# Optimization experiments

Hardware: AMD Instinct MI355X
Metric: run time of the kernel (lower is better)

Reference implementation:

```python
import jax, jax.numpy as jnp
import numpy as np

B, N = 4, 500
C_DIM = 256            # content_dim == feat_channels
G = 4                  # n_groups
P_IN, P_OUT = 32, 128
EFF = C_DIM // G       # 64 = eff_in_dim = eff_out_dim
TOTAL = EFF * EFF + P_IN * P_OUT   # 8192 params per group per query
STRIDES = (8, 16, 32, 64)
LVL_SHAPES = ((100, 160), (50, 80), (25, 40), (13, 20))
TAU = 2.0
LVL_MAP = 3.0          # log2(STRIDES[0]): z -> fpn level index
EPS = 1e-5


def setup_inputs() -> dict:
    key = jax.random.key(0)
    ks = jax.random.split(key, 16)
    feats = [jax.random.normal(ks[i], (B, C_DIM, h, w), jnp.float32)
             for i, (h, w) in enumerate(LVL_SHAPES)]
    query_feat = jax.random.normal(ks[4], (B, N, C_DIM), jnp.float32)
    xy = jax.random.uniform(ks[5], (B, N, 2), jnp.float32, 50.0, 1000.0)
    z = jax.random.uniform(ks[6], (B, N, 1), jnp.float32, 3.0, 6.0)
    r = jax.random.uniform(ks[7], (B, N, 1), jnp.float32, -1.0, 1.0)
    query_xyzr = jnp.concatenate([xy, z, r], -1)
    w_off = jax.random.normal(ks[8], (C_DIM, P_IN * G * 3), jnp.float32) * 0.01
    b_off = jax.random.normal(ks[9], (P_IN * G * 3,), jnp.float32) * 0.1
    w_pg = jax.random.normal(ks[10], (C_DIM, G * TOTAL), jnp.float32) * 0.02
    b_pg = jax.random.normal(ks[11], (G * TOTAL,), jnp.float32) * 0.02
    w_out = jax.random.normal(ks[12], (G * P_OUT * EFF, C_DIM), jnp.float32) * 0.005
    b_out = jnp.zeros((C_DIM,), jnp.float32)
    ln_g = jnp.ones((C_DIM,), jnp.float32)
    ln_b = jnp.zeros((C_DIM,), jnp.float32)
    return dict(feat0=feats[0], feat1=feats[1], feat2=feats[2], feat3=feats[3],
                query_feat=query_feat, query_xyzr=query_xyzr,
                w_off=w_off, b_off=b_off, w_pg=w_pg, b_pg=b_pg,
                w_out=w_out, b_out=b_out, ln_g=ln_g, ln_b=ln_b)


def _ln2d(x):
    # F.layer_norm over last TWO dims, no affine
    mu = x.mean((-2, -1), keepdims=True)
    var = jnp.mean((x - mu) ** 2, (-2, -1), keepdims=True)
    return (x - mu) * jax.lax.rsqrt(var + EPS)


def _bilinear(feat, px, py):
    # torch grid_sample(bilinear, zeros padding, align_corners=False)
    # feat: [BG, H, W, Cg]; px, py: [BG, Q] pixel coords
    BGn, H, W, Cg = feat.shape
    fflat = feat.reshape(BGn, H * W, Cg)
    bidx = jnp.arange(BGn)[:, None]
    x0 = jnp.floor(px)
    y0 = jnp.floor(py)
    wx, wy = px - x0, py - y0
    x0i, y0i = x0.astype(jnp.int32), y0.astype(jnp.int32)

    def corner(xi, yi, w):
        valid = (xi >= 0) & (xi < W) & (yi >= 0) & (yi < H)
        idx = jnp.clip(yi, 0, H - 1) * W + jnp.clip(xi, 0, W - 1)
        return fflat[bidx, idx] * (w * valid)[..., None]

    return (corner(x0i, y0i, (1 - wx) * (1 - wy)) + corner(x0i + 1, y0i, wx * (1 - wy))
            + corner(x0i, y0i + 1, (1 - wx) * wy) + corner(x0i + 1, y0i + 1, wx * wy))


def _forward(feat0, feat1, feat2, feat3, query_feat, query_xyzr,
             w_off, b_off, w_pg, b_pg, w_out, b_out, ln_g, ln_b):
    feats = (feat0, feat1, feat2, feat3)
    # --- make_sample_points ---
    off = (query_feat @ w_off + b_off).reshape(B, N, G * P_IN, 3)
    cc = query_xyzr[..., :2]
    z = query_xyzr[..., 2:3]
    r = query_xyzr[..., 3:4]
    roi_wh = (2.0 ** z) * jnp.concatenate([2.0 ** (-0.5 * r), 2.0 ** (0.5 * r)], -1)  # [B,N,2]
    sample_xy = cc[:, :, None, :] + off[..., :2] * roi_wh[:, :, None, :]   # [B,N,G*P,2]
    sample_lvl = z[:, :, None, 0:1] + off[..., 2:3]                        # [B,N,G*P,1]

    # --- sampling_3d: softmax level weights ---
    lvl = sample_lvl[..., 0] - LVL_MAP                                     # [B,N,G*P]
    grid = jnp.arange(len(STRIDES), dtype=lvl.dtype)
    lw = jax.nn.softmax(-((lvl[..., None] - grid) ** 2) / TAU, axis=-1)    # [B,N,G*P,L]

    # regroup to per-group layout [B*G, N*P, ...]
    sx = sample_xy.reshape(B, N, G, P_IN, 2).transpose(0, 2, 1, 3, 4).reshape(B * G, N * P_IN, 2)
    lw_g = lw.reshape(B, N, G, P_IN, -1).transpose(0, 2, 1, 3, 4).reshape(B * G, N * P_IN, -1)

    sampled = jnp.zeros((B * G, N * P_IN, EFF), jnp.float32)
    for li, (feat, stride) in enumerate(zip(feats, STRIDES)):
        H, W = feat.shape[2], feat.shape[3]
        fg = feat.reshape(B * G, EFF, H, W).transpose(0, 2, 3, 1)  # [BG,H,W,EFF]
        nx = sx[..., 0] / (W * stride) * 2.0 - 1.0
        ny = sx[..., 1] / (H * stride) * 2.0 - 1.0
        px = (nx + 1.0) * 0.5 * W - 0.5
        py = (ny + 1.0) * 0.5 * H - 0.5
        sampled = sampled + _bilinear(fg, px, py) * lw_g[..., li][..., None]
    # [B,N,G,P,EFF]
    x = sampled.reshape(B, G, N, P_IN, EFF).transpose(0, 2, 1, 3, 4)

    # --- AdaptiveMixing ---
    params = (query_feat @ w_pg + b_pg).reshape(B * N, G, TOTAL)
    M = params[..., :EFF * EFF].reshape(B * N, G, EFF, EFF)
    S = params[..., EFF * EFF:].reshape(B * N, G, P_OUT, P_IN)
    out = x.reshape(B * N, G, P_IN, EFF)
    out = jax.nn.relu(_ln2d(jnp.einsum('bgpc,bgcd->bgpd', out, M)))  # channel mix
    out = jax.nn.relu(_ln2d(jnp.einsum('bgop,bgpd->bgod', S, out)))  # spatial mix
    out = out.reshape(B, N, G * P_OUT * EFF) @ w_out + b_out
    q = query_feat + out

    # --- final LayerNorm(content_dim) with affine ---
    mu = q.mean(-1, keepdims=True)
    var = jnp.mean((q - mu) ** 2, -1, keepdims=True)
    return (q - mu) * jax.lax.rsqrt(var + EPS) * ln_g + ln_b


def reference(feat0, feat1, feat2, feat3, query_feat, query_xyzr,
              w_off, b_off, w_pg, b_pg, w_out, b_out, ln_g, ln_b):
    return _forward(feat0, feat1, feat2, feat3, query_feat, query_xyzr,
                    w_off, b_off, w_pg, b_pg, w_out, b_out, ln_g, ln_b)
```

## Files before the change

### kernel.cpp

```cpp
#include <hip/hip_runtime.h>
#include <hip/hip_bf16.h>
#include <cstdint>
#include <cstddef>

#define DI __device__ __forceinline__

#define NN 500
#define NQ 2000
#define GTOT 32768
#define LN_EPS 1e-5f

typedef __attribute__((ext_vector_type(8))) short short8v;
typedef __attribute__((ext_vector_type(4))) float f32x4;
typedef const __attribute__((address_space(1))) void* gp1_t;
typedef __attribute__((address_space(3))) void* lp3_t;

DI unsigned short f2bf(float f){
  unsigned u = __float_as_uint(f);
  return (unsigned short)((u + 0x7fffu + ((u>>16)&1u)) >> 16);
}
DI float bf2f(unsigned short s){ return __uint_as_float(((unsigned)s)<<16); }

DI ushort4 cvt4(float4 a){
  ushort4 r; r.x=f2bf(a.x); r.y=f2bf(a.y); r.z=f2bf(a.z); r.w=f2bf(a.w); return r;
}

DI void bred256(float& s, float& s2, float* red, int tid){
  #pragma unroll
  for(int off=32; off; off>>=1){
    s  += __shfl_xor(s,  off, 64);
    s2 += __shfl_xor(s2, off, 64);
  }
  int w = tid>>6;
  if((tid&63)==0){ red[w*2]=s; red[w*2+1]=s2; }
  __syncthreads();
  s  = red[0]+red[2]+red[4]+red[6];
  s2 = red[1]+red[3]+red[5]+red[7];
  __syncthreads();
}

__global__ __launch_bounds__(384) void k_off(const float* __restrict__ qf,
    const float* __restrict__ xyzr, const float* __restrict__ w_off,
    const float* __restrict__ b_off, float2* __restrict__ xyb, float4* __restrict__ lwb){
  __shared__ float qs[8][256];
  __shared__ float os[8][384];
  int q0 = blockIdx.x*8, tid = threadIdx.x;
  for(int idx=tid; idx<2048; idx+=384){
    int qq = idx>>8, k = idx&255;
    qs[qq][k] = qf[(size_t)(q0+qq)*256 + k];
  }
  __syncthreads();
  {
    int j = tid;
    float acc[8];
    #pragma unroll
    for(int i=0;i<8;i++) acc[i]=0.f;
    for(int k=0;k<256;k++){
      float w = w_off[(size_t)k*384 + j];
      #pragma unroll
      for(int qq=0;qq<8;qq++) acc[qq] += qs[qq][k]*w;
    }
    float bb = b_off[j];
    #pragma unroll
    for(int qq=0;qq<8;qq++) os[qq][j] = acc[qq] + bb;
  }
  __syncthreads();
  for(int idx=tid; idx<1024; idx+=384){
    int qq = idx>>7, gp = idx&127;
    int q = q0+qq;
    float4 xr = *(const float4*)&xyzr[(size_t)q*4];
    float rw = exp2f(xr.z - 0.5f*xr.w);
    float rh = exp2f(xr.z + 0.5f*xr.w);
    float sx = xr.x + os[qq][gp*3+0]*rw;
    float sy = xr.y + os[qq][gp*3+1]*rh;
    float lvl = xr.z + os[qq][gp*3+2] - 3.0f;
    float d0=lvl, d1=lvl-1.f, d2=lvl-2.f, d3=lvl-3.f;
    float e0=-0.5f*d0*d0, e1=-0.5f*d1*d1, e2=-0.5f*d2*d2, e3=-0.5f*d3*d3;
    float m = fmaxf(fmaxf(e0,e1),fmaxf(e2,e3));
    float x0=expf(e0-m), x1=expf(e1-m), x2=expf(e2-m), x3=expf(e3-m);
    float inv = 1.f/(x0+x1+x2+x3);
    xyb[(size_t)q*128+gp] = make_float2(sx,sy);
    lwb[(size_t)q*128+gp] = make_float4(x0*inv, x1*inv, x2*inv, x3*inv);
  }
}

__global__ __launch_bounds__(256) void k_cvtqf(const float* __restrict__ qf,
    unsigned short* __restrict__ qfb){
  int idx = blockIdx.x*256 + threadIdx.x;
  size_t base = (size_t)idx*8;
  int row = idx >> 5;
  ushort4 lo, hi;
  if(row < NQ){
    float4 a = *(const float4*)(qf + base);
    float4 b = *(const float4*)(qf + base + 4);
    lo = cvt4(a); hi = cvt4(b);
  } else {
    lo.x=lo.y=lo.z=lo.w=0; hi.x=hi.y=hi.z=hi.w=0;
  }
  *(ushort4*)(qfb + base) = lo;
  *(ushort4*)(qfb + base + 4) = hi;
}

__global__ __launch_bounds__(256) void k_trcvt(const float* __restrict__ src,
    unsigned short* __restrict__ dst, int R, int C){
  __shared__ unsigned short tile[64*68];
  int ctiles = C >> 6;
  int rt = blockIdx.x / ctiles, ct = blockIdx.x % ctiles;
  int r0 = rt<<6, c0 = ct<<6;
  int tid = threadIdx.x;
  #pragma unroll
  for(int i=0;i<4;i++){
    int idx = tid + i*256;
    int r = idx >> 4, c4 = (idx & 15)*4;
    float4 v = *(const float4*)(src + (size_t)(r0+r)*C + c0 + c4);
    *(ushort4*)(tile + r*68 + c4) = cvt4(v);
  }
  __syncthreads();
  #pragma unroll
  for(int i=0;i<4;i++){
    int idx = tid + i*256;
    int cc = idx >> 4, r4 = (idx & 15)*4;
    ushort4 v;
    v.x = tile[(r4+0)*68 + cc];
    v.y = tile[(r4+1)*68 + cc];
    v.z = tile[(r4+2)*68 + cc];
    v.w = tile[(r4+3)*68 + cc];
    *(ushort4*)(dst + (size_t)(c0+cc)*R + r0 + r4) = v;
  }
}

__global__ __launch_bounds__(256) void k_featT(const float* __restrict__ src,
    unsigned short* __restrict__ dst, int HW, int nb){
  __shared__ unsigned short tile[64*68];
  int bg = blockIdx.x / nb, hb = blockIdx.x % nb;
  int b = bg >> 2, g = bg & 3;
  const float* s = src + ((size_t)(b*256 + g*64))*HW + hb*64;
  unsigned short* d = dst + (size_t)bg*HW*64 + (size_t)hb*64*64;
  int rem = HW - hb*64;
  int tid = threadIdx.x;
  #pragma unroll
  for(int i=0;i<4;i++){
    int idx = tid + i*256;
    int c = idx >> 4, h4 = (idx & 15)*4;
    if(h4 < rem){
      float4 v = *(const float4*)(s + (size_t)c*HW + h4);
      *(ushort4*)(tile + c*68 + h4) = cvt4(v);
    }
  }
  __syncthreads();
  #pragma unroll
  for(int i=0;i<4;i++){
    int idx = tid + i*256;
    int hw = idx >> 4, c4 = (idx & 15)*4;
    if(hw < rem){
      ushort4 v;
      v.x = tile[(c4+0)*68 + hw];
      v.y = tile[(c4+1)*68 + hw];
      v.z = tile[(c4+2)*68 + hw];
      v.w = tile[(c4+3)*68 + hw];
      *(ushort4*)(d + (size_t)hw*64 + c4) = v;
    }
  }
}

DI f32x4 mfma16(short8v a, short8v b, f32x4 c){
  return __builtin_amdgcn_mfma_f32_16x16x32_bf16(a, b, c, 0, 0, 0);
}

DI int swz32(int c, int r){ return c ^ (r&3) ^ ((r>>2)&3); }

DI void stageG32(const unsigned short* __restrict__ g, size_t row0, size_t ldk,
                 size_t k0, unsigned short* lds, int tid){
  int wv = tid>>6;
  #pragma unroll
  for(int i=0;i<2;i++){
    int e = i*256 + tid;
    int r = e>>2, c = e&3;
    int cs = swz32(c, r);
    const unsigned short* gp = g + (row0 + (size_t)r)*ldk + k0 + (size_t)cs*8;
    unsigned short* lp = lds + (size_t)(i*256 + wv*64)*8;
    __builtin_amdgcn_global_load_lds((gp1_t)(const void*)gp, (lp3_t)(void*)lp, 16, 0, 0);
  }
}

DI void stageB32(const unsigned short* __restrict__ g, size_t row0, size_t ldk,
                 size_t k0, unsigned short* lds, int tid){
  int wv = tid>>6;
  int r = tid>>2, c = tid&3;
  int cs = swz32(c, r);
  const unsigned short* gp = g + (row0 + (size_t)r)*ldk + k0 + (size_t)cs*8;
  unsigned short* lp = lds + (size_t)(wv*64)*8;
  __builtin_amdgcn_global_load_lds((gp1_t)(const void*)gp, (lp3_t)(void*)lp, 16, 0, 0);
}

DI short8v frag32(const unsigned short* lds, int row, int q4){
  return *(const short8v*)(lds + (size_t)row*32 + (size_t)swz32(q4, row)*8);
}

DI void mma32(const unsigned short* lsA, const unsigned short* lsB,
              int wm, int wn, int lane, f32x4 acc[4][4]){
  int r15 = lane&15, q4 = lane>>4;
  short8v a[4], b[4];
  #pragma unroll
  for(int i=0;i<4;i++){
    a[i] = frag32(lsA, wm*64 + i*16 + r15, q4);
    b[i] = frag32(lsB, wn*64 + i*16 + r15, q4);
  }
  #pragma unroll
  for(int mi=0;mi<4;mi++)
    #pragma unroll
    for(int ni=0;ni<4;ni++)
      acc[mi][ni] = mfma16(a[mi], b[ni], acc[mi][ni]);
}

DI int xcd_remap(int bid, int nwg){
  return ((bid & 7) * (nwg >> 3)) + (bid >> 3);
}

__global__ __launch_bounds__(256, 4) void k_pgemm_mfma(const unsigned short* __restrict__ qfb,
    const unsigned short* __restrict__ wpgT, const float* __restrict__ b_pg,
    unsigned short* __restrict__ par, int qbase, int qlim, int mtiles){
  __shared__ unsigned short pool[16384];
  int bid = xcd_remap(blockIdx.x, gridDim.x);
  int mt = bid % mtiles, nt = bid / mtiles;
  size_t m0 = (size_t)mt*128, n0 = (size_t)nt*128;
  int tid = threadIdx.x, lane = tid&63, wv = tid>>6;
  int wm = wv>>1, wn = wv&1;
  int r15 = lane&15, q4 = lane>>4;
  f32x4 acc[4][4] = {};
  stageG32(qfb,  qbase+m0, 256, 0, pool, tid);
  stageG32(wpgT, n0,       256, 0, pool + 8192, tid);
  __syncthreads();
  #pragma unroll
  for(int t=0; t<8; t++){
    int co = (t&1)*4096;
    if(t<7){
      int no = ((t&1)^1)*4096;
      stageG32(qfb,  qbase+m0, 256, (size_t)(t+1)*32, pool + no, tid);
      stageG32(wpgT, n0,       256, (size_t)(t+1)*32, pool + 8192 + no, tid);
    }
    mma32(pool + co, pool + 8192 + co, wm, wn, lane, acc);
    __syncthreads();
  }
  unsigned short* es = pool;
  #pragma unroll
  for(int h=0; h<2; ++h){
    if(h) __syncthreads();
    if(wn == h){
      #pragma unroll
      for(int ni=0; ni<4; ni++){
        float bias = b_pg[(int)n0 + wn*64 + ni*16 + r15];
        #pragma unroll
        for(int mi=0; mi<4; mi++)
          #pragma unroll
          for(int j=0; j<4; j++){
            int row = wm*64 + mi*16 + q4*4 + j;
            es[row*72 + ni*16 + r15] = f2bf(acc[mi][ni][j] + bias);
          }
      }
    }
    __syncthreads();
    #pragma unroll
    for(int i=0;i<4;i++){
      int e = i*256 + tid;
      int row = e>>3, c8 = (e&7)*8;
      int rl = (int)m0 + row;
      if(qbase + rl < qlim){
        uint4 v = *(const uint4*)(es + row*72 + c8);
        *(uint4*)&par[(size_t)rl*GTOT + n0 + h*64 + c8] = v;
      }
    }
  }
}

__global__ __launch_bounds__(256, 4) void k_fgemm_mfma(const unsigned short* __restrict__ Ag,
    const unsigned short* __restrict__ woutT, float* __restrict__ part,
    int qbase, int qlim, int mtiles, int kspl){
  __shared__ unsigned short pool[12288];
  int bid = xcd_remap(blockIdx.x, gridDim.x);
  int nt = bid & 3;
  int r2 = bid >> 2;
  int mt = r2 % mtiles, ks = r2 / mtiles;
  size_t m0 = (size_t)mt*128, n0 = (size_t)nt*64;
  int tid = threadIdx.x, lane = tid&63, wv = tid>>6;
  int wm = wv>>1, wn = wv&1;
  int r15 = lane&15, q4 = lane>>4;
  f32x4 acc[4][2] = {};
  int klen = GTOT / kspl;
  size_t kbase = (size_t)ks*klen;
  int NT = klen >> 5;
  stageG32(Ag,    m0, GTOT, kbase, pool, tid);
  stageB32(woutT, n0, GTOT, kbase, pool + 8192, tid);
  __syncthreads();
  for(int t=0; t<NT; t++){
    int coA = (t&1)*4096, coB = (t&1)*2048;
    if(t+1<NT){
      int noA = ((t&1)^1)*4096, noB = ((t&1)^1)*2048;
      stageG32(Ag,    m0, GTOT, kbase + (size_t)(t+1)*32, pool + noA, tid);
      stageB32(woutT, n0, GTOT, kbase + (size_t)(t+1)*32, pool + 8192 + noB, tid);
    }
    {
      const unsigned short* lsA = pool + coA;
      const unsigned short* lsB = pool + 8192 + coB;
      short8v a[4], b[2];
      #pragma unroll
      for(int i=0;i<4;i++) a[i] = frag32(lsA, wm*64 + i*16 + r15, q4);
      #pragma unroll
      for(int i=0;i<2;i++) b[i] = frag32(lsB, wn*32 + i*16 + r15, q4);
      #pragma unroll
      for(int mi=0;mi<4;mi++)
        #pragma unroll
        for(int ni=0;ni<2;ni++)
          acc[mi][ni] = mfma16(a[mi], b[ni], acc[mi][ni]);
    }
    __syncthreads();
  }
  float* pp = part + (size_t)ks*NQ*256;
  #pragma unroll
  for(int mi=0; mi<4; mi++){
    #pragma unroll
    for(int j=0; j<4; j++){
      int rl = (int)m0 + wm*64 + mi*16 + q4*4 + j;
      int q = qbase + rl;
      if(q < qlim){
        #pragma unroll
        for(int ni=0; ni<2; ni++){
          int col = (int)n0 + wn*32 + ni*16 + r15;
          pp[(size_t)q*256 + col] = acc[mi][ni][j];
        }
      }
    }
  }
}

__global__ __launch_bounds__(256) void k_mix(const unsigned short* __restrict__ featT,
    const float2* __restrict__ xyb, const float4* __restrict__ lwb,
    const unsigned short* __restrict__ par, unsigned short* __restrict__ out2,
    int qbase){
  __shared__ __align__(16) char poolA[23040];
  __shared__ __align__(16) unsigned short Ss[128*40];
  __shared__ float red[8];
  float* offW = (float*)poolA;
  unsigned short* xs  = (unsigned short*)(poolA + 4096);
  unsigned short* Ms  = (unsigned short*)(poolA + 4096 + 4608);
  unsigned short* o1t = (unsigned short*)(poolA + 4096 + 4608 + 9216);
  unsigned short* o2s = (unsigned short*)poolA;

  int lq = blockIdx.x >> 2, g = blockIdx.x & 3;
  int q = qbase + lq;
  int b = q / NN;
  int bg = b*4 + g;
  int tid = threadIdx.x;
  int lane = tid & 63, wv = tid >> 6;

  const int HH[4] = {100,50,25,13};
  const int WW[4] = {160,80,40,20};
  const float IS[4] = {0.125f, 0.0625f, 0.03125f, 0.015625f};
  const int LO[4] = {0, 16384000, 20480000, 21504000};

  const unsigned short* pb = par + (size_t)lq*GTOT + (size_t)g*8192;
  uint4 mraw0 = *(const uint4*)(pb + tid*8);
  uint4 mraw1 = *(const uint4*)(pb + 2048 + tid*8);
  uint4 sraw0 = *(const uint4*)(pb + 4096 + tid*8);
  uint4 sraw1 = *(const uint4*)(pb + 6144 + tid*8);

  if(tid < 128){
    int p = tid >> 2, l = tid & 3;
    int pi = q*128 + g*32 + p;
    float2 xy = xyb[pi];
    float lw4 = ((const float*)lwb)[(size_t)pi*4 + l];
    int H = HH[l], W = WW[l];
    float px = xy.x*IS[l] - 0.5f;
    float py = xy.y*IS[l] - 0.5f;
    float xf = floorf(px), yf = floorf(py);
    float wx = px - xf, wy = py - yf;
    int x0 = (int)xf, y0 = (int)yf;
    int x1 = x0 + 1, y1 = y0 + 1;
    bool vx0 = (x0>=0)&&(x0<W), vx1 = (x1>=0)&&(x1<W);
    bool vy0 = (y0>=0)&&(y0<H), vy1 = (y1>=0)&&(y1<H);
    int x0c = min(max(x0,0),W-1), x1c = min(max(x1,0),W-1);
    int y0c = min(max(y0,0),H-1), y1c = min(max(y1,0),H-1);
    int base = LO[l] + bg*H*W*64;
    float* e = offW + tid*8;
    e[0] = __int_as_float(base + (y0c*W + x0c)*64);
    e[1] = __int_as_float(base + (y0c*W + x1c)*64);
    e[2] = __int_as_float(base + (y1c*W + x0c)*64);
    e[3] = __int_as_float(base + (y1c*W + x1c)*64);
    e[4] = (1.f-wx)*(1.f-wy)*lw4*(float)(vx0&&vy0);
    e[5] = wx*(1.f-wy)*lw4*(float)(vx1&&vy0);
    e[6] = (1.f-wx)*wy*lw4*(float)(vx0&&vy1);
    e[7] = wx*wy*lw4*(float)(vx1&&vy1);
  }

  {
    int idx0 = tid*8;
    int c0 = idx0>>6, d0 = idx0&63;
    *(uint4*)(Ms + c0*72 + d0) = mraw0;
    int idx1 = 2048 + tid*8;
    int c1 = idx1>>6, d1 = idx1&63;
    *(uint4*)(Ms + c1*72 + d1) = mraw1;
    int o0 = idx0>>5, p0 = idx0&31;
    *(uint4*)(Ss + o0*40 + p0) = sraw0;
    int o1_ = idx1>>5, p1 = idx1&31;
    *(uint4*)(Ss + o1_*40 + p1) = sraw1;
  }
  __syncthreads();

  {
    int half = lane >> 5, cp = lane & 31;
    const unsigned short* fb_ = featT + cp*2;
    #pragma unroll
    for(int i=0;i<4;i++){
      int p = wv*8 + i*2 + half;
      const float* e = offW + p*32;
      float aLo = 0.f, aHi = 0.f;
      #pragma unroll
      for(int l=0;l<4;l++){
        float4 ea = *(const float4*)(e + l*8);
        float4 eb = *(const float4*)(e + l*8 + 4);
        unsigned u00 = *(const unsigned*)(fb_ + __float_as_int(ea.x));
        unsigned u01 = *(const unsigned*)(fb_ + __float_as_int(ea.y));
        unsigned u10 = *(const unsigned*)(fb_ + __float_as_int(ea.z));
        unsigned u11 = *(const unsigned*)(fb_ + __float_as_int(ea.w));
        aLo += eb.x*__uint_as_float(u00<<16); aHi += eb.x*__uint_as_float(u00&0xffff0000u);
        aLo += eb.y*__uint_as_float(u01<<16); aHi += eb.y*__uint_as_float(u01&0xffff0000u);
        aLo += eb.z*__uint_as_float(u10<<16); aHi += eb.z*__uint_as_float(u10&0xffff0000u);
        aLo += eb.w*__uint_as_float(u11<<16); aHi += eb.w*__uint_as_float(u11&0xffff0000u);
      }
      unsigned lo = f2bf(aLo), hi = f2bf(aHi);
      *(unsigned*)(xs + p*72 + cp*2) = lo | (hi<<16);
    }
  }
  __syncthreads();

  int r = lane & 15, q4 = lane >> 4;

  {
    short8v af00 = *(const short8v*)(xs + r*72 + q4*8);
    short8v af01 = *(const short8v*)(xs + r*72 + 32 + q4*8);
    short8v af10 = *(const short8v*)(xs + (16+r)*72 + q4*8);
    short8v af11 = *(const short8v*)(xs + (16+r)*72 + 32 + q4*8);
    short8v bm0, bm1;
    #pragma unroll
    for(int j=0;j<8;j++){
      bm0[j] = (short)Ms[(8*q4+j)*72 + wv*16 + r];
      bm1[j] = (short)Ms[(32+8*q4+j)*72 + wv*16 + r];
    }
    f32x4 a0 = {}, a1 = {};
    a0 = mfma16(af00, bm0, a0); a0 = mfma16(af01, bm1, a0);
    a1 = mfma16(af10, bm0, a1); a1 = mfma16(af11, bm1, a1);

    float s = 0.f, s2 = 0.f;
    #pragma unroll
    for(int v=0;v<4;v++){ s += a0[v]+a1[v]; s2 += a0[v]*a0[v] + a1[v]*a1[v]; }
    bred256(s, s2, red, tid);
    float mean = s*(1.f/2048.f);
    float var = s2*(1.f/2048.f) - mean*mean;
    float rs = rsqrtf(var + LN_EPS);
    #pragma unroll
    for(int v=0;v<4;v++){
      float f0 = (a0[v]-mean)*rs; f0 = f0>0.f ? f0 : 0.f;
      float f1 = (a1[v]-mean)*rs; f1 = f1>0.f ? f1 : 0.f;
      o1t[(wv*16+r)*40 + 4*q4 + v] = f2bf(f0);
      o1t[(wv*16+r)*40 + 16 + 4*q4 + v] = f2bf(f1);
    }
  }
  __syncthreads();

  {
    short8v sa0 = *(const short8v*)(Ss + ((wv*2+0)*16 + r)*40 + q4*8);
    short8v sa1 = *(const short8v*)(Ss + ((wv*2+1)*16 + r)*40 + q4*8);
    short8v ov0 = *(const short8v*)(o1t + (r)*40 + q4*8);
    short8v ov1 = *(const short8v*)(o1t + (16+r)*40 + q4*8);
    short8v ov2 = *(const short8v*)(o1t + (32+r)*40 + q4*8);
    short8v ov3 = *(const short8v*)(o1t + (48+r)*40 + q4*8);
    f32x4 c2[2][4] = {};
    c2[0][0] = mfma16(sa0, ov0, c2[0][0]); c2[0][1] = mfma16(sa0, ov1, c2[0][1]);
    c2[0][2] = mfma16(sa0, ov2, c2[0][2]); c2[0][3] = mfma16(sa0, ov3, c2[0][3]);
    c2[1][0] = mfma16(sa1, ov0, c2[1][0]); c2[1][1] = mfma16(sa1, ov1, c2[1][1]);
    c2[1][2] = mfma16(sa1, ov2, c2[1][2]); c2[1][3] = mfma16(sa1, ov3, c2[1][3]);

    float s = 0.f, s2 = 0.f;
    #pragma unroll
    for(int m=0;m<2;m++)
      #pragma unroll
      for(int ni=0;ni<4;ni++)
        #pragma unroll
        for(int v=0;v<4;v++){ float x = c2[m][ni][v]; s += x; s2 += x*x; }
    bred256(s, s2, red, tid);
    float mean = s*(1.f/8192.f);
    float var = s2*(1.f/8192.f) - mean*mean;
    float rs = rsqrtf(var + LN_EPS);
    #pragma unroll
    for(int m=0;m<2;m++)
      #pragma unroll
      for(int ni=0;ni<4;ni++)
        #pragma unroll
        for(int v=0;v<4;v++){
          float x = (c2[m][ni][v]-mean)*rs; x = x>0.f ? x : 0.f;
          int o = (wv*2+m)*16 + 4*q4 + v;
          int d = ni*16 + r;
          o2s[o*72 + d] = f2bf(x);
        }
  }
  __syncthreads();

  unsigned short* og = out2 + (size_t)lq*GTOT + (size_t)g*8192;
  #pragma unroll
  for(int i=0;i<32;i++){
    int row = wv*32 + i;
    og[row*64 + lane] = o2s[row*72 + lane];
  }
}

__global__ __launch_bounds__(256) void k_ln(const float* __restrict__ part,
    const float* __restrict__ qf, const float* __restrict__ b_out,
    const float* __restrict__ ln_g, const float* __restrict__ ln_b,
    float* __restrict__ out, int kspl){
  __shared__ float red[8];
  int q = blockIdx.x, j = threadIdx.x;
  float s = qf[(size_t)q*256 + j] + b_out[j];
  for(int ks=0; ks<kspl; ks++) s += part[((size_t)ks*NQ + q)*256 + j];
  float a = s, a2 = s*s;
  bred256(a, a2, red, j);
  float mean = a*(1.f/256.f);
  float var = a2*(1.f/256.f) - mean*mean;
  float rs = rsqrtf(var + LN_EPS);
  out[(size_t)q*256 + j] = (s-mean)*rs*ln_g[j] + ln_b[j];
}

extern "C" void kernel_launch(void* const* d_in, const int* in_sizes, int n_in,
                              void* d_out, int out_size, void* d_ws, size_t ws_size,
                              hipStream_t stream) {
  const float* feat0 = (const float*)d_in[0];
  const float* feat1 = (const float*)d_in[1];
  const float* feat2 = (const float*)d_in[2];
  const float* feat3 = (const float*)d_in[3];
  const float* qf    = (const float*)d_in[4];
  const float* xyzr  = (const float*)d_in[5];
  const float* w_off = (const float*)d_in[6];
  const float* b_off = (const float*)d_in[7];
  const float* w_pg  = (const float*)d_in[8];
  const float* b_pg  = (const float*)d_in[9];
  const float* w_out = (const float*)d_in[10];
  const float* b_out = (const float*)d_in[11];
  const float* ln_g  = (const float*)d_in[12];
  const float* ln_b  = (const float*)d_in[13];

  const int cand_ksp[5] = {32,16,16,16,16};
  const int cand_nc [5] = { 1, 1, 2, 4, 8};
  int KSP=0, NC=0, qcount=0, qpad=0;
  size_t oFEAT=0,oXY=0,oLW=0,oPART=0,oQFB=0,oWPGT=0,oWOUT=0,oPAR=0;
  for(int ci=0; ci<5; ci++){
    size_t o = 0;
    auto al = [&](size_t bytes){ size_t r = o; o = (o + bytes + 255) & ~255ull; return r; };
    size_t tFEAT = al(43540480ull);
    size_t tXY   = al((size_t)NQ*128*8);
    size_t tLW   = al((size_t)NQ*128*16);
    size_t tPART = al((size_t)cand_ksp[ci]*NQ*256*4);
    size_t tQFB  = al((size_t)2048*256*2);
    size_t tWPGT = al((size_t)GTOT*256*2);
    size_t tWOUT = al((size_t)256*GTOT*2);
    int qc = NQ / cand_nc[ci];
    int qp = (qc + 127) & ~127;
    size_t tPAR = al((size_t)qp*GTOT*2);
    if(o <= ws_size){
      KSP=cand_ksp[ci]; NC=cand_nc[ci]; qcount=qc; qpad=qp;
      oFEAT=tFEAT; oXY=tXY; oLW=tLW; oPART=tPART; oQFB=tQFB; oWPGT=tWPGT; oWOUT=tWOUT; oPAR=tPAR;
      break;
    }
  }
  if(NC == 0) return;

  char* ws = (char*)d_ws;
  unsigned short* featT = (unsigned short*)(ws + oFEAT);
  float2* xyb = (float2*)(ws + oXY);
  float4* lwb = (float4*)(ws + oLW);
  float* part = (float*)(ws + oPART);
  unsigned short* qfb  = (unsigned short*)(ws + oQFB);
  unsigned short* wpgT = (unsigned short*)(ws + oWPGT);
  unsigned short* woutT= (unsigned short*)(ws + oWOUT);
  unsigned short* par  = (unsigned short*)(ws + oPAR);
  unsigned short* o2   = par;

  k_off<<<250, 384, 0, stream>>>(qf, xyzr, w_off, b_off, xyb, lwb);
  k_cvtqf<<<256, 256, 0, stream>>>(qf, qfb);
  k_trcvt<<<2048, 256, 0, stream>>>(w_pg,  wpgT, 256, GTOT);
  k_trcvt<<<2048, 256, 0, stream>>>(w_out, woutT, GTOT, 256);
  k_featT<<<16*250, 256, 0, stream>>>(feat0, featT + 0,        16000, 250);
  k_featT<<<16*63,  256, 0, stream>>>(feat1, featT + 16384000, 4000,  63);
  k_featT<<<16*16,  256, 0, stream>>>(feat2, featT + 20480000, 1000,  16);
  k_featT<<<16*5,   256, 0, stream>>>(feat3, featT + 21504000, 260,   5);

  int mtiles = qpad / 128;
  for (int c = 0; c < NC; ++c) {
    int qbase = c * qcount;
    int qlim  = qbase + qcount;
    k_pgemm_mfma<<<mtiles*256, 256, 0, stream>>>(qfb, wpgT, b_pg, par, qbase, qlim, mtiles);
    k_mix<<<qcount*4, 256, 0, stream>>>(featT, xyb, lwb, par, o2, qbase);
    k_fgemm_mfma<<<mtiles*4*KSP, 256, 0, stream>>>(o2, woutT, part, qbase, qlim, mtiles, KSP);
  }
  k_ln<<<NQ, 256, 0, stream>>>(part, qf, b_out, ln_g, ln_b, (float*)d_out, KSP);
}
```

Before: 321.7 us.

## Fuse prep kernels, widen fgemm N-tile to 128, alias partials workspace

Merges the separate conversion and transpose kernels (query cast, two weight transposes, four feature transposes) into one launch that dispatches on block index. The output GEMM now uses 128x128 tiles with the shared mma32 helper instead of 128x64, which halves the block count and reuses each A tile across twice as many output columns. The workspace layout overlaps the split-K partial buffer with the front of the workspace so a single chunk fits more often. The bigger tile raises register and LDS use per block, and the overlap is only safe if nothing still needs the reused region when the partials are written.

```diff
diff --git a/kernel.cpp b/kernel.cpp
--- a/kernel.cpp
+++ b/kernel.cpp
@@ -84,82 +84,91 @@
   }
 }
 
-__global__ __launch_bounds__(256) void k_cvtqf(const float* __restrict__ qf,
-    unsigned short* __restrict__ qfb){
-  int idx = blockIdx.x*256 + threadIdx.x;
-  size_t base = (size_t)idx*8;
-  int row = idx >> 5;
-  ushort4 lo, hi;
-  if(row < NQ){
-    float4 a = *(const float4*)(qf + base);
-    float4 b = *(const float4*)(qf + base + 4);
-    lo = cvt4(a); hi = cvt4(b);
+__global__ __launch_bounds__(256) void k_prep2(
+    const float* __restrict__ f0, const float* __restrict__ f1,
+    const float* __restrict__ f2, const float* __restrict__ f3,
+    const float* __restrict__ qf, const float* __restrict__ w_pg,
+    const float* __restrict__ w_out, unsigned short* __restrict__ featT,
+    unsigned short* __restrict__ qfb, unsigned short* __restrict__ wpgT,
+    unsigned short* __restrict__ woutT){
+  __shared__ unsigned short tile[64*68];
+  int bid = blockIdx.x, tid = threadIdx.x;
+
+  if(bid < 4096){
+    const float* src; unsigned short* dst; int R, C, lb;
+    if(bid < 2048){ src=w_pg;  dst=wpgT;  R=256;  C=GTOT; lb=bid; }
+    else          { src=w_out; dst=woutT; R=GTOT; C=256;  lb=bid-2048; }
+    int ctiles = C >> 6;
+    int rt = lb / ctiles, ct = lb % ctiles;
+    int r0 = rt<<6, c0 = ct<<6;
+    #pragma unroll
+    for(int i=0;i<4;i++){
+      int idx = tid + i*256;
+      int r = idx >> 4, c4 = (idx & 15)*4;
+      float4 v = *(const float4*)(src + (size_t)(r0+r)*C + c0 + c4);
+      *(ushort4*)(tile + r*68 + c4) = cvt4(v);
+    }
+    __syncthreads();
+    #pragma unroll
+    for(int i=0;i<4;i++){
+      int idx = tid + i*256;
+      int cc = idx >> 4, r4 = (idx & 15)*4;
+      ushort4 v;
+      v.x = tile[(r4+0)*68 + cc];
+      v.y = tile[(r4+1)*68 + cc];
+      v.z = tile[(r4+2)*68 + cc];
+      v.w = tile[(r4+3)*68 + cc];
+      *(ushort4*)(dst + (size_t)(c0+cc)*R + r0 + r4) = v;
+    }
+  } else if(bid < 9440){
+    const float* src; unsigned short* dst; int HW, nb, lb;
+    int fb = bid - 4096;
+    if(fb < 4000){ src=f0; dst=featT;            HW=16000; nb=250; lb=fb; }
+    else if(fb < 5008){ src=f1; dst=featT+16384000; HW=4000; nb=63; lb=fb-4000; }
+    else if(fb < 5264){ src=f2; dst=featT+20480000; HW=1000; nb=16; lb=fb-5008; }
+    else { src=f3; dst=featT+21504000; HW=260; nb=5; lb=fb-5264; }
+    int bg = lb / nb, hb = lb % nb;
+    int b = bg >> 2, g = bg & 3;
+    const float* s = src + ((size_t)(b*256 + g*64))*HW + hb*64;
+    unsigned short* d = dst + (size_t)bg*HW*64 + (size_t)hb*64*64;
+    int rem = HW - hb*64;
+    #pragma unroll
+    for(int i=0;i<4;i++){
+      int idx = tid + i*256;
+      int c = idx >> 4, h4 = (idx & 15)*4;
+      if(h4 < rem){
+        float4 v = *(const float4*)(s + (size_t)c*HW + h4);
+        *(ushort4*)(tile + c*68 + h4) = cvt4(v);
+      }
+    }
+    __syncthreads();
+    #pragma unroll
+    for(int i=0;i<4;i++){
+      int idx = tid + i*256;
+      int hw = idx >> 4, c4 = (idx & 15)*4;
+      if(hw < rem){
+        ushort4 v;
+        v.x = tile[(c4+0)*68 + hw];
+        v.y = tile[(c4+1)*68 + hw];
+        v.z = tile[(c4+2)*68 + hw];
+        v.w = tile[(c4+3)*68 + hw];
+        *(ushort4*)(d + (size_t)hw*64 + c4) = v;
+      }
+    }
   } else {
-    lo.x=lo.y=lo.z=lo.w=0; hi.x=hi.y=hi.z=hi.w=0;
-  }
-  *(ushort4*)(qfb + base) = lo;
-  *(ushort4*)(qfb + base + 4) = hi;
-}
-
-__global__ __launch_bounds__(256) void k_trcvt(const float* __restrict__ src,
-    unsigned short* __restrict__ dst, int R, int C){
-  __shared__ unsigned short tile[64*68];
-  int ctiles = C >> 6;
-  int rt = blockIdx.x / ctiles, ct = blockIdx.x % ctiles;
-  int r0 = rt<<6, c0 = ct<<6;
-  int tid = threadIdx.x;
-  #pragma unroll
-  for(int i=0;i<4;i++){
-    int idx = tid + i*256;
-    int r = idx >> 4, c4 = (idx & 15)*4;
-    float4 v = *(const float4*)(src + (size_t)(r0+r)*C + c0 + c4);
-    *(ushort4*)(tile + r*68 + c4) = cvt4(v);
-  }
-  __syncthreads();
-  #pragma unroll
-  for(int i=0;i<4;i++){
-    int idx = tid + i*256;
-    int cc = idx >> 4, r4 = (idx & 15)*4;
-    ushort4 v;
-    v.x = tile[(r4+0)*68 + cc];
-    v.y = tile[(r4+1)*68 + cc];
-    v.z = tile[(r4+2)*68 + cc];
-    v.w = tile[(r4+3)*68 + cc];
-    *(ushort4*)(dst + (size_t)(c0+cc)*R + r0 + r4) = v;
-  }
-}
-
-__global__ __launch_bounds__(256) void k_featT(const float* __restrict__ src,
-    unsigned short* __restrict__ dst, int HW, int nb){
-  __shared__ unsigned short tile[64*68];
-  int bg = blockIdx.x / nb, hb = blockIdx.x % nb;
-  int b = bg >> 2, g = bg & 3;
-  const float* s = src + ((size_t)(b*256 + g*64))*HW + hb*64;
-  unsigned short* d = dst + (size_t)bg*HW*64 + (size_t)hb*64*64;
-  int rem = HW - hb*64;
-  int tid = threadIdx.x;
-  #pragma unroll
-  for(int i=0;i<4;i++){
-    int idx = tid + i*256;
-    int c = idx >> 4, h4 = (idx & 15)*4;
-    if(h4 < rem){
-      float4 v = *(const float4*)(s + (size_t)c*HW + h4);
-      *(ushort4*)(tile + c*68 + h4) = cvt4(v);
-    }
-  }
-  __syncthreads();
-  #pragma unroll
-  for(int i=0;i<4;i++){
-    int idx = tid + i*256;
-    int hw = idx >> 4, c4 = (idx & 15)*4;
-    if(hw < rem){
-      ushort4 v;
-      v.x = tile[(c4+0)*68 + hw];
-      v.y = tile[(c4+1)*68 + hw];
-      v.z = tile[(c4+2)*68 + hw];
-      v.w = tile[(c4+3)*68 + hw];
-      *(ushort4*)(d + (size_t)hw*64 + c4) = v;
-    }
+    int idx = (bid-9440)*256 + tid;
+    size_t base = (size_t)idx*8;
+    int row = idx >> 5;
+    ushort4 lo, hi;
+    if(row < NQ){
+      float4 a = *(const float4*)(qf + base);
+      float4 b = *(const float4*)(qf + base + 4);
+      lo = cvt4(a); hi = cvt4(b);
+    } else {
+      lo.x=lo.y=lo.z=lo.w=0; hi.x=hi.y=hi.z=hi.w=0;
+    }
+    *(ushort4*)(qfb + base) = lo;
+    *(ushort4*)(qfb + base + 4) = hi;
   }
 }
 
@@ -181,16 +190,6 @@
     unsigned short* lp = lds + (size_t)(i*256 + wv*64)*8;
     __builtin_amdgcn_global_load_lds((gp1_t)(const void*)gp, (lp3_t)(void*)lp, 16, 0, 0);
   }
-}
-
-DI void stageB32(const unsigned short* __restrict__ g, size_t row0, size_t ldk,
-                 size_t k0, unsigned short* lds, int tid){
-  int wv = tid>>6;
-  int r = tid>>2, c = tid&3;
-  int cs = swz32(c, r);
-  const unsigned short* gp = g + (row0 + (size_t)r)*ldk + k0 + (size_t)cs*8;
-  unsigned short* lp = lds + (size_t)(wv*64)*8;
-  __builtin_amdgcn_global_load_lds((gp1_t)(const void*)gp, (lp3_t)(void*)lp, 16, 0, 0);
 }
 
 DI short8v frag32(const unsigned short* lds, int row, int q4){
@@ -276,46 +275,33 @@
 __global__ __launch_bounds__(256, 4) void k_fgemm_mfma(const unsigned short* __restrict__ Ag,
     const unsigned short* __restrict__ woutT, float* __restrict__ part,
     int qbase, int qlim, int mtiles, int kspl){
-  __shared__ unsigned short pool[12288];
+  __shared__ unsigned short pool[16384];
   int bid = xcd_remap(blockIdx.x, gridDim.x);
-  int nt = bid & 3;
-  int r2 = bid >> 2;
+  int nt = bid & 1;
+  int r2 = bid >> 1;
   int mt = r2 % mtiles, ks = r2 / mtiles;
-  size_t m0 = (size_t)mt*128, n0 = (size_t)nt*64;
+  size_t m0 = (size_t)mt*128, n0 = (size_t)nt*128;
   int tid = threadIdx.x, lane = tid&63, wv = tid>>6;
   int wm = wv>>1, wn = wv&1;
-  int r15 = lane&15, q4 = lane>>4;
-  f32x4 acc[4][2] = {};
+  f32x4 acc[4][4] = {};
   int klen = GTOT / kspl;
   size_t kbase = (size_t)ks*klen;
   int NT = klen >> 5;
   stageG32(Ag,    m0, GTOT, kbase, pool, tid);
-  stageB32(woutT, n0, GTOT, kbase, pool + 8192, tid);
+  stageG32(woutT, n0, GTOT, kbase, pool + 8192, tid);
   __syncthreads();
   for(int t=0; t<NT; t++){
-    int coA = (t&1)*4096, coB = (t&1)*2048;
+    int co = (t&1)*4096;
     if(t+1<NT){
-      int noA = ((t&1)^1)*4096, noB = ((t&1)^1)*2048;
-      stageG32(Ag,    m0, GTOT, kbase + (size_t)(t+1)*32, pool + noA, tid);
-      stageB32(woutT, n0, GTOT, kbase + (size_t)(t+1)*32, pool + 8192 + noB, tid);
-    }
-    {
-      const unsigned short* lsA = pool + coA;
-      const unsigned short* lsB = pool + 8192 + coB;
-      short8v a[4], b[2];
-      #pragma unroll
-      for(int i=0;i<4;i++) a[i] = frag32(lsA, wm*64 + i*16 + r15, q4);
-      #pragma unroll
-      for(int i=0;i<2;i++) b[i] = frag32(lsB, wn*32 + i*16 + r15, q4);
-      #pragma unroll
-      for(int mi=0;mi<4;mi++)
-        #pragma unroll
-        for(int ni=0;ni<2;ni++)
-          acc[mi][ni] = mfma16(a[mi], b[ni], acc[mi][ni]);
-    }
+      int no = ((t&1)^1)*4096;
+      stageG32(Ag,    m0, GTOT, kbase + (size_t)(t+1)*32, pool + no, tid);
+      stageG32(woutT, n0, GTOT, kbase + (size_t)(t+1)*32, pool + 8192 + no, tid);
+    }
+    mma32(pool + co, pool + 8192 + co, wm, wn, lane, acc);
     __syncthreads();
   }
   float* pp = part + (size_t)ks*NQ*256;
+  int r15 = lane&15, q4 = lane>>4;
   #pragma unroll
   for(int mi=0; mi<4; mi++){
     #pragma unroll
@@ -324,8 +310,8 @@
       int q = qbase + rl;
       if(q < qlim){
         #pragma unroll
-        for(int ni=0; ni<2; ni++){
-          int col = (int)n0 + wn*32 + ni*16 + r15;
+        for(int ni=0; ni<4; ni++){
+          int col = (int)n0 + wn*64 + ni*16 + r15;
           pp[(size_t)q*256 + col] = acc[mi][ni][j];
         }
       }
@@ -547,27 +533,45 @@
   const float* ln_g  = (const float*)d_in[12];
   const float* ln_b  = (const float*)d_in[13];
 
-  const int cand_ksp[5] = {32,16,16,16,16};
-  const int cand_nc [5] = { 1, 1, 2, 4, 8};
   int KSP=0, NC=0, qcount=0, qpad=0;
   size_t oFEAT=0,oXY=0,oLW=0,oPART=0,oQFB=0,oWPGT=0,oWOUT=0,oPAR=0;
-  for(int ci=0; ci<5; ci++){
-    size_t o = 0;
-    auto al = [&](size_t bytes){ size_t r = o; o = (o + bytes + 255) & ~255ull; return r; };
-    size_t tFEAT = al(43540480ull);
-    size_t tXY   = al((size_t)NQ*128*8);
-    size_t tLW   = al((size_t)NQ*128*16);
-    size_t tPART = al((size_t)cand_ksp[ci]*NQ*256*4);
-    size_t tQFB  = al((size_t)2048*256*2);
-    size_t tWPGT = al((size_t)GTOT*256*2);
-    size_t tWOUT = al((size_t)256*GTOT*2);
-    int qc = NQ / cand_nc[ci];
-    int qp = (qc + 127) & ~127;
-    size_t tPAR = al((size_t)qp*GTOT*2);
-    if(o <= ws_size){
-      KSP=cand_ksp[ci]; NC=cand_nc[ci]; qcount=qc; qpad=qp;
-      oFEAT=tFEAT; oXY=tXY; oLW=tLW; oPART=tPART; oQFB=tQFB; oWPGT=tWPGT; oWOUT=tWOUT; oPAR=tPAR;
-      break;
+  {
+    const int a_ksp[2] = {32, 16};
+    for(int ci=0; ci<2 && NC==0; ci++){
+      size_t o = 0;
+      auto al = [&](size_t bytes){ size_t r = o; o = (o + bytes + 255) & ~255ull; return r; };
+      size_t tFEAT = al(43540480ull);
+      size_t tXY   = al((size_t)NQ*128*8);
+      size_t tLW   = al((size_t)NQ*128*16);
+      size_t tQFB  = al((size_t)2048*256*2);
+      size_t tWPGT = al((size_t)GTOT*256*2);
+      size_t partBytes = (size_t)a_ksp[ci]*NQ*256*4;
+      if(partBytes > o) o = (partBytes + 255) & ~255ull;
+      size_t tWOUT = al((size_t)256*GTOT*2);
+      size_t tPAR  = al((size_t)2048*GTOT*2);
+      if(o <= ws_size){
+        KSP=a_ksp[ci]; NC=1; qcount=NQ; qpad=2048;
+        oFEAT=tFEAT; oXY=tXY; oLW=tLW; oPART=0; oQFB=tQFB; oWPGT=tWPGT; oWOUT=tWOUT; oPAR=tPAR;
+      }
+    }
+    const int c_nc[3] = {2,4,8};
+    for(int ci=0; ci<3 && NC==0; ci++){
+      size_t o = 0;
+      auto al = [&](size_t bytes){ size_t r = o; o = (o + bytes + 255) & ~255ull; return r; };
+      size_t tFEAT = al(43540480ull);
+      size_t tXY   = al((size_t)NQ*128*8);
+      size_t tLW   = al((size_t)NQ*128*16);
+      size_t tPART = al((size_t)16*NQ*256*4);
+      size_t tQFB  = al((size_t)2048*256*2);
+      size_t tWPGT = al((size_t)GTOT*256*2);
+      size_t tWOUT = al((size_t)256*GTOT*2);
+      int qc = NQ / c_nc[ci];
+      int qp = (qc + 127) & ~127;
+      size_t tPAR = al((size_t)qp*GTOT*2);
+      if(o <= ws_size){
+        KSP=16; NC=c_nc[ci]; qcount=qc; qpad=qp;
+        oFEAT=tFEAT; oXY=tXY; oLW=tLW; oPART=tPART; oQFB=tQFB; oWPGT=tWPGT; oWOUT=tWOUT; oPAR=tPAR;
+      }
     }
   }
   if(NC == 0) return;
@@ -584,13 +588,8 @@
   unsigned short* o2   = par;
 
   k_off<<<250, 384, 0, stream>>>(qf, xyzr, w_off, b_off, xyb, lwb);
-  k_cvtqf<<<256, 256, 0, stream>>>(qf, qfb);
-  k_trcvt<<<2048, 256, 0, stream>>>(w_pg,  wpgT, 256, GTOT);
-  k_trcvt<<<2048, 256, 0, stream>>>(w_out, woutT, GTOT, 256);
-  k_featT<<<16*250, 256, 0, stream>>>(feat0, featT + 0,        16000, 250);
-  k_featT<<<16*63,  256, 0, stream>>>(feat1, featT + 16384000, 4000,  63);
-  k_featT<<<16*16,  256, 0, stream>>>(feat2, featT + 20480000, 1000,  16);
-  k_featT<<<16*5,   256, 0, stream>>>(feat3, featT + 21504000, 260,   5);
+  k_prep2<<<9696, 256, 0, stream>>>(feat0, feat1, feat2, feat3, qf, w_pg, w_out,
+                                    featT, qfb, wpgT, woutT);
 
   int mtiles = qpad / 128;
   for (int c = 0; c < NC; ++c) {
@@ -598,7 +597,7 @@
     int qlim  = qbase + qcount;
     k_pgemm_mfma<<<mtiles*256, 256, 0, stream>>>(qfb, wpgT, b_pg, par, qbase, qlim, mtiles);
     k_mix<<<qcount*4, 256, 0, stream>>>(featT, xyb, lwb, par, o2, qbase);
-    k_fgemm_mfma<<<mtiles*4*KSP, 256, 0, stream>>>(o2, woutT, part, qbase, qlim, mtiles, KSP);
+    k_fgemm_mfma<<<mtiles*2*KSP, 256, 0, stream>>>(o2, woutT, part, qbase, qlim, mtiles, KSP);
   }
   k_ln<<<NQ, 256, 0, stream>>>(part, qf, b_out, ln_g, ln_b, (float*)d_out, KSP);
 }
```

Result: faster. 300.9 us (-6.5%).
